# Performance work log

Measured on AMD Instinct MI355X. Metric: run time of the kernel, lower is better.

The kernel has to match this reference:

```python
import jax, jax.numpy as jnp
import numpy as np

HIDDEN = 2048
NUM_HEADS = 16
NUM_KV_HEADS = 4
HEAD_DIM = 128
ROPE_BASE = 10000.0


def apply_rope(x):
    # x: [B, H, S, D]; standard half-split RoPE
    B, H, S, D = x.shape
    half = D // 2
    inv_freq = 1.0 / (ROPE_BASE ** (jnp.arange(half, dtype=jnp.float32) / half))
    ang = jnp.arange(S, dtype=jnp.float32)[:, None] * inv_freq[None, :]  # [S, half]
    cos = jnp.cos(ang).astype(x.dtype)
    sin = jnp.sin(ang).astype(x.dtype)
    x1, x2 = x[..., :half], x[..., half:]
    return jnp.concatenate([x1 * cos - x2 * sin, x1 * sin + x2 * cos], axis=-1)


def setup_inputs() -> dict:
    key = jax.random.key(0)
    ks = jax.random.split(key, 6)
    B, S = 2, 2048
    sd = 1.0 / np.sqrt(HIDDEN)
    x = jax.random.normal(ks[0], (B, S, HIDDEN), dtype=jnp.float32)
    wq = jax.random.normal(ks[1], (NUM_HEADS * HEAD_DIM, HIDDEN), dtype=jnp.float32) * sd
    wk = jax.random.normal(ks[2], (NUM_KV_HEADS * HEAD_DIM, HIDDEN), dtype=jnp.float32) * sd
    wv = jax.random.normal(ks[3], (NUM_KV_HEADS * HEAD_DIM, HIDDEN), dtype=jnp.float32) * sd
    wo = jax.random.normal(ks[4], (HIDDEN, NUM_HEADS * HEAD_DIM), dtype=jnp.float32) * sd
    key_weights = jnp.ones((NUM_HEADS,), dtype=jnp.float32)
    return {"x": x, "wq": wq, "wk": wk, "wv": wv, "wo": wo, "key_weights": key_weights}


def reference(x, wq, wk, wv, wo, key_weights):
    B, S, _ = x.shape
    g = NUM_HEADS // NUM_KV_HEADS
    scale = HEAD_DIM ** -0.5
    # projections -> [B, H, S, D]
    q = (x @ wq.T).reshape(B, S, NUM_HEADS, HEAD_DIM).transpose(0, 2, 1, 3)
    k = (x @ wk.T).reshape(B, S, NUM_KV_HEADS, HEAD_DIM).transpose(0, 2, 1, 3)
    v = (x @ wv.T).reshape(B, S, NUM_KV_HEADS, HEAD_DIM).transpose(0, 2, 1, 3)
    q = apply_rope(q)
    k = apply_rope(k)
    # GQA expansion (repeat_interleave over head dim)
    k = jnp.repeat(k, g, axis=1)
    v = jnp.repeat(v, g, axis=1)
    # per-head key scaling fused into K
    k = k * key_weights[None, :, None, None]
    scores = jnp.einsum("bhqd,bhkd->bhqk", q, k) * scale
    causal = jnp.triu(jnp.ones((S, S), dtype=bool), k=1)
    scores = jnp.where(causal, -jnp.inf, scores)
    attn = jax.nn.softmax(scores, axis=-1)
    out = jnp.einsum("bhqk,bhkd->bhqd", attn, v)
    out = out.transpose(0, 2, 1, 3).reshape(B, S, NUM_HEADS * HEAD_DIM)
    return out @ wo.T
```

## Files before the change

### kernel.cpp

```cpp
#include <hip/hip_runtime.h>

#define S_LEN 2048
#define HID 2048
#define NH 16
#define HD 128
#define QKV_N 3072
#define KCOL 2048
#define VCOL 2560

typedef unsigned short ushort_t;
using bf16x8 = __attribute__((ext_vector_type(8))) __bf16;
using f32x4 = __attribute__((ext_vector_type(4))) float;
using ushort8 = __attribute__((ext_vector_type(8))) unsigned short;
using ushort4v = __attribute__((ext_vector_type(4))) unsigned short;

__device__ __forceinline__ unsigned short f2bf(float f) {
  unsigned int u = __float_as_uint(f);
  unsigned int r = u + 0x7FFFu + ((u >> 16) & 1u);
  return (unsigned short)(r >> 16);
}
__device__ __forceinline__ float bf2f(unsigned short h) {
  return __uint_as_float(((unsigned int)h) << 16);
}

__device__ __forceinline__ void gload_lds16(const ushort_t* g, ushort_t* lds) {
  __builtin_amdgcn_global_load_lds(
      (const __attribute__((address_space(1))) unsigned int*)g,
      (__attribute__((address_space(3))) unsigned int*)lds, 16, 0, 0);
}

__global__ void cast_bf16_kernel(const float* __restrict__ in, ushort_t* __restrict__ out, int n4) {
  int i = blockIdx.x * 256 + threadIdx.x;
  if (i >= n4) return;
  float4 v = reinterpret_cast<const float4*>(in)[i];
  ushort4v o;
  o.x = f2bf(v.x); o.y = f2bf(v.y); o.z = f2bf(v.z); o.w = f2bf(v.w);
  reinterpret_cast<ushort4v*>(out)[i] = o;
}

__global__ void rope_table_kernel(float* __restrict__ cosT, float* __restrict__ sinT) {
  int i = blockIdx.x * 256 + threadIdx.x;
  if (i >= S_LEN * 64) return;
  int s = i >> 6, j = i & 63;
  float inv = __expf(-(float)j * (9.210340371976184f / 64.0f));
  float ang = (float)s * inv;
  float sv, cv;
  sincosf(ang, &sv, &cv);
  cosT[i] = cv;
  sinT[i] = sv;
}

__global__ void rope_apply_kernel(ushort_t* __restrict__ base, const float* __restrict__ cosT,
                                  const float* __restrict__ sinT, const float* __restrict__ kw,
                                  int stride, int lognh, float scale, int useKw, int n) {
  int idx = blockIdx.x * 256 + threadIdx.x;
  if (idx >= n) return;
  int row = idx >> lognh;
  int p = idx & ((1 << lognh) - 1);
  int h = p >> 6, j = p & 63;
  int s = row & (S_LEN - 1);
  float c = cosT[(s << 6) + j];
  float sn = sinT[(s << 6) + j];
  long a = (long)row * stride + h * HD;
  float x1 = bf2f(base[a + j]);
  float x2 = bf2f(base[a + j + 64]);
  float wsc = useKw ? (scale * kw[h]) : scale;
  base[a + j] = f2bf((x1 * c - x2 * sn) * wsc);
  base[a + j + 64] = f2bf((x1 * sn + x2 * c) * wsc);
}

__global__ __launch_bounds__(256) void transpose_v_kernel(const ushort_t* __restrict__ qkv,
                                                          ushort_t* __restrict__ vt) {
  __shared__ ushort_t T[64][76];
  int bid = blockIdx.x;
  int dd = bid & 7;
  int tt = bid >> 3;
  int tid = threadIdx.x;
#pragma unroll
  for (int it = 0; it < 2; ++it) {
    int c = tid + it * 256;
    int i = c >> 3, j8 = c & 7;
    ushort8 v = *reinterpret_cast<const ushort8*>(
        qkv + (long)(tt * 64 + i) * QKV_N + VCOL + dd * 64 + j8 * 8);
    *reinterpret_cast<ushort8*>(&T[i][j8 * 8]) = v;
  }
  __syncthreads();
#pragma unroll
  for (int it = 0; it < 2; ++it) {
    int c = tid + it * 256;
    int jd = c >> 3, sc = c & 7;
    ushort8 o;
#pragma unroll
    for (int e = 0; e < 8; ++e) o[e] = T[sc * 8 + e][jd];
    int token = tt * 64 + sc * 8;
    int b = token >> 11, s = token & (S_LEN - 1);
    int vd = dd * 64 + jd;
    *reinterpret_cast<ushort8*>(vt + ((long)(b * 512 + vd) << 11) + s) = o;
  }
}

__device__ __forceinline__ void store_c(ushort_t* p, float v) { *p = f2bf(v); }
__device__ __forceinline__ void store_c(float* p, float v) { *p = v; }

template <typename OT>
__global__ __launch_bounds__(256) void gemm_bt_kernel(const ushort_t* __restrict__ A,
                                                      const ushort_t* __restrict__ W,
                                                      OT* __restrict__ C, int M, int N, int K) {
  __shared__ ushort_t As[128 * 32];
  __shared__ ushort_t Bs[128 * 32];
  const int tid = threadIdx.x;
  const int l = tid & 63, w = tid >> 6;
  const int wr = w >> 1, wc = w & 1;
  const int r = l & 15, g = l >> 4;
  const long arow0 = (long)blockIdx.y * 128;
  const long brow0 = (long)blockIdx.x * 128;

  f32x4 acc[4][4] = {};

  const int c0 = tid, c1 = tid + 256;
  const ushort_t* a_src0 = A + (arow0 + (c0 >> 2)) * K + ((c0 & 3) << 3);
  const ushort_t* a_src1 = A + (arow0 + (c1 >> 2)) * K + ((c1 & 3) << 3);
  const ushort_t* b_src0 = W + (brow0 + (c0 >> 2)) * K + ((c0 & 3) << 3);
  const ushort_t* b_src1 = W + (brow0 + (c1 >> 2)) * K + ((c1 & 3) << 3);
  ushort_t* a_dst0 = &As[c0 * 8];
  ushort_t* a_dst1 = &As[c1 * 8];
  ushort_t* b_dst0 = &Bs[c0 * 8];
  ushort_t* b_dst1 = &Bs[c1 * 8];

  for (int kk = 0; kk < K; kk += 32) {
    gload_lds16(a_src0 + kk, a_dst0);
    gload_lds16(a_src1 + kk, a_dst1);
    gload_lds16(b_src0 + kk, b_dst0);
    gload_lds16(b_src1 + kk, b_dst1);
    __syncthreads();
    bf16x8 af[4], bw[4];
#pragma unroll
    for (int mi = 0; mi < 4; ++mi)
      af[mi] = *reinterpret_cast<const bf16x8*>(&As[(wr * 64 + mi * 16 + r) * 32 + g * 8]);
#pragma unroll
    for (int ni = 0; ni < 4; ++ni)
      bw[ni] = *reinterpret_cast<const bf16x8*>(&Bs[(wc * 64 + ni * 16 + r) * 32 + g * 8]);
#pragma unroll
    for (int mi = 0; mi < 4; ++mi)
#pragma unroll
      for (int ni = 0; ni < 4; ++ni)
        acc[mi][ni] = __builtin_amdgcn_mfma_f32_16x16x32_bf16(af[mi], bw[ni], acc[mi][ni], 0, 0, 0);
    __syncthreads();
  }

#pragma unroll
  for (int mi = 0; mi < 4; ++mi)
#pragma unroll
    for (int ni = 0; ni < 4; ++ni) {
      int col = (int)brow0 + wc * 64 + ni * 16 + r;
#pragma unroll
      for (int j = 0; j < 4; ++j) {
        int row = (int)arow0 + wr * 64 + mi * 16 + g * 4 + j;
        store_c(&C[(long)row * N + col], acc[mi][ni][j]);
      }
    }
}

__global__ __launch_bounds__(256) void flash_attn_kernel(const ushort_t* __restrict__ qkv,
                                                         const ushort_t* __restrict__ Vt,
                                                         ushort_t* __restrict__ AO) {
  __shared__ ushort_t Ks[64 * 128];
  __shared__ ushort_t Vts[128 * 64];
  __shared__ ushort_t Ps[4][16 * 68];

  const int bid = blockIdx.x;
  const int pr = bid & 15;
  const int h = (bid >> 4) & 15;
  const int b = bid >> 8;
  const int tid = threadIdx.x;
  const int l = tid & 63, w = tid >> 6;
  const int r = l & 15, g = l >> 4;
  const int kvh = h >> 2;

  const ushort_t* Qb = qkv + (long)b * S_LEN * QKV_N + h * HD;
  const ushort_t* Kb = qkv + (long)b * S_LEN * QKV_N + KCOL + kvh * HD;
  const ushort_t* Vb = Vt + ((long)(b * 512 + kvh * HD) << 11);

  for (int pi = 0; pi < 2; ++pi) {
    const int qt = pi ? (31 - pr) : pr;
    const int qg = qt * 64 + w * 16;
    const long qrow0 = (long)b * S_LEN + qg;

    bf16x8 qa[4];
#pragma unroll
    for (int ks = 0; ks < 4; ++ks)
      qa[ks] = *reinterpret_cast<const bf16x8*>(Qb + (long)(qg + r) * QKV_N + ks * 32 + g * 8);

    f32x4 acc[8] = {};
    float mrow[4], lrow[4];
#pragma unroll
    for (int j = 0; j < 4; ++j) { mrow[j] = -1e30f; lrow[j] = 0.f; }

    for (int kv = 0; kv <= qt; ++kv) {
      __syncthreads();
#pragma unroll
      for (int i = 0; i < 4; ++i) {
        int c = tid + i * 256;
        int krow = c >> 4, cc = c & 15;
        int scc = cc ^ (krow & 7);
        gload_lds16(Kb + (long)(kv * 64 + krow) * QKV_N + scc * 8, &Ks[c * 8]);
      }
#pragma unroll
      for (int i = 0; i < 4; ++i) {
        int c = tid + i * 256;
        int vrow = c >> 3, cc = c & 7;
        int scc = cc ^ (vrow & 7);
        gload_lds16(Vb + ((long)vrow << 11) + kv * 64 + scc * 8, &Vts[c * 8]);
      }
      __syncthreads();

      f32x4 s[4] = {};
#pragma unroll
      for (int ks = 0; ks < 4; ++ks) {
        bf16x8 kf[4];
#pragma unroll
        for (int ni = 0; ni < 4; ++ni) {
          int n = ni * 16 + r;
          int chunk = (ks * 4 + g) ^ (n & 7);
          kf[ni] = *reinterpret_cast<const bf16x8*>(
              reinterpret_cast<const char*>(Ks) + n * 256 + chunk * 16);
        }
#pragma unroll
        for (int ni = 0; ni < 4; ++ni)
          s[ni] = __builtin_amdgcn_mfma_f32_16x16x32_bf16(qa[ks], kf[ni], s[ni], 0, 0, 0);
      }
      if (kv == qt) {
#pragma unroll
        for (int ni = 0; ni < 4; ++ni) {
          int key = kv * 64 + ni * 16 + r;
#pragma unroll
          for (int j = 0; j < 4; ++j) {
            int rowq = qg + g * 4 + j;
            if (key > rowq) s[ni][j] = -1e30f;
          }
        }
      }
#pragma unroll
      for (int j = 0; j < 4; ++j) {
        float mx = fmaxf(fmaxf(s[0][j], s[1][j]), fmaxf(s[2][j], s[3][j]));
        mx = fmaxf(mx, __shfl_xor(mx, 1));
        mx = fmaxf(mx, __shfl_xor(mx, 2));
        mx = fmaxf(mx, __shfl_xor(mx, 4));
        mx = fmaxf(mx, __shfl_xor(mx, 8));
        float mo = mrow[j];
        float mn = fmaxf(mo, mx);
        float ef = __expf(mo - mn);
        mrow[j] = mn;
        float psum = 0.f;
#pragma unroll
        for (int ni = 0; ni < 4; ++ni) {
          float p = __expf(s[ni][j] - mn);
          s[ni][j] = p;
          psum += p;
        }
        lrow[j] = lrow[j] * ef + psum;
#pragma unroll
        for (int ni = 0; ni < 8; ++ni) acc[ni][j] *= ef;
      }
#pragma unroll
      for (int ni = 0; ni < 4; ++ni)
#pragma unroll
        for (int j = 0; j < 4; ++j)
          Ps[w][(g * 4 + j) * 68 + ni * 16 + r] = f2bf(s[ni][j]);
#pragma unroll
      for (int ks2 = 0; ks2 < 2; ++ks2) {
        bf16x8 pa = *reinterpret_cast<const bf16x8*>(&Ps[w][r * 68 + ks2 * 32 + g * 8]);
#pragma unroll
        for (int ni = 0; ni < 8; ++ni) {
          int d = ni * 16 + r;
          int chunk = (ks2 * 4 + g) ^ (d & 7);
          bf16x8 vf = *reinterpret_cast<const bf16x8*>(
              reinterpret_cast<const char*>(Vts) + d * 128 + chunk * 16);
          acc[ni] = __builtin_amdgcn_mfma_f32_16x16x32_bf16(pa, vf, acc[ni], 0, 0, 0);
        }
      }
    }

#pragma unroll
    for (int j = 0; j < 4; ++j) {
      float lt = lrow[j];
      lt += __shfl_xor(lt, 1);
      lt += __shfl_xor(lt, 2);
      lt += __shfl_xor(lt, 4);
      lt += __shfl_xor(lt, 8);
      float inv = 1.0f / lt;
#pragma unroll
      for (int ni = 0; ni < 8; ++ni) acc[ni][j] *= inv;
    }
#pragma unroll
    for (int ni = 0; ni < 8; ++ni) {
      int col = h * HD + ni * 16 + r;
#pragma unroll
      for (int j = 0; j < 4; ++j) {
        long row = qrow0 + g * 4 + j;
        AO[row * HID + col] = f2bf(acc[ni][j]);
      }
    }
    __syncthreads();
  }
}

extern "C" void kernel_launch(void* const* d_in, const int* in_sizes, int n_in,
                              void* d_out, int out_size, void* d_ws, size_t ws_size,
                              hipStream_t stream) {
  const float* x = (const float*)d_in[0];
  const float* wq = (const float*)d_in[1];
  const float* wk = (const float*)d_in[2];
  const float* wv = (const float*)d_in[3];
  const float* wo = (const float*)d_in[4];
  const float* kw = (const float*)d_in[5];
  float* out = (float*)d_out;

  ushort_t* ws = (ushort_t*)d_ws;
  ushort_t* xb = ws;
  ushort_t* qkv = xb + 8388608;
  ushort_t* vt = qkv + 12582912;
  ushort_t* wqkv = vt + 2097152;
  float* cosT = (float*)(wqkv + 6291456);
  float* sinT = cosT + S_LEN * 64;

  cast_bf16_kernel<<<8192, 256, 0, stream>>>(x, xb, 2097152);
  cast_bf16_kernel<<<4096, 256, 0, stream>>>(wq, wqkv, 1048576);
  cast_bf16_kernel<<<1024, 256, 0, stream>>>(wk, wqkv + 2048 * 2048, 262144);
  cast_bf16_kernel<<<1024, 256, 0, stream>>>(wv, wqkv + 2560 * 2048, 262144);
  rope_table_kernel<<<512, 256, 0, stream>>>(cosT, sinT);

  gemm_bt_kernel<ushort_t><<<dim3(24, 32), 256, 0, stream>>>(xb, wqkv, qkv, 4096, QKV_N, 2048);

  rope_apply_kernel<<<16384, 256, 0, stream>>>(qkv, cosT, sinT, kw, QKV_N, 10,
                                               0.08838834764831845f, 1, 4194304);
  rope_apply_kernel<<<4096, 256, 0, stream>>>(qkv + KCOL, cosT, sinT, kw, QKV_N, 8,
                                              1.0f, 0, 1048576);

  transpose_v_kernel<<<512, 256, 0, stream>>>(qkv, vt);

  ushort_t* wob = wqkv;
  cast_bf16_kernel<<<4096, 256, 0, stream>>>(wo, wob, 1048576);

  flash_attn_kernel<<<512, 256, 0, stream>>>(qkv, vt, xb);

  gemm_bt_kernel<float><<<dim3(16, 32), 256, 0, stream>>>(xb, wob, out, 4096, 2048, 2048);
}
```

Before: 349.4 us.

## Double-buffer K/V tiles in flash attention and remap blocks across XCDs

Stages K and V tiles into two LDS buffers so the next tile's global-to-LDS load is issued before computing on the current tile, leaving one barrier per iteration instead of two. It also replaces the padded P scratch with an XOR-swizzled layout and remaps the block index so related heads and batches are grouped per XCD for L2 reuse. The extra buffers raise LDS use, which may reduce the number of resident blocks per CU.

```diff
diff --git a/kernel.cpp b/kernel.cpp
--- a/kernel.cpp
+++ b/kernel.cpp
@@ -161,17 +161,38 @@
     }
 }
 
+__device__ __forceinline__ void stage_tile(const ushort_t* __restrict__ Kb,
+                                           const ushort_t* __restrict__ Vb, int kv,
+                                           ushort_t* __restrict__ KsBuf,
+                                           ushort_t* __restrict__ VtsBuf, int tid) {
+#pragma unroll
+  for (int i = 0; i < 4; ++i) {
+    int c = tid + i * 256;
+    int krow = c >> 4, cc = c & 15;
+    int scc = cc ^ (krow & 7);
+    gload_lds16(Kb + (long)(kv * 64 + krow) * QKV_N + scc * 8, &KsBuf[c * 8]);
+  }
+#pragma unroll
+  for (int i = 0; i < 4; ++i) {
+    int c = tid + i * 256;
+    int vrow = c >> 3, cc = c & 7;
+    int scc = cc ^ (vrow & 7);
+    gload_lds16(Vb + ((long)vrow << 11) + kv * 64 + scc * 8, &VtsBuf[c * 8]);
+  }
+}
+
 __global__ __launch_bounds__(256) void flash_attn_kernel(const ushort_t* __restrict__ qkv,
                                                          const ushort_t* __restrict__ Vt,
                                                          ushort_t* __restrict__ AO) {
-  __shared__ ushort_t Ks[64 * 128];
-  __shared__ ushort_t Vts[128 * 64];
-  __shared__ ushort_t Ps[4][16 * 68];
-
-  const int bid = blockIdx.x;
-  const int pr = bid & 15;
-  const int h = (bid >> 4) & 15;
-  const int b = bid >> 8;
+  __shared__ ushort_t Ks[2][64 * 128];
+  __shared__ ushort_t Vts[2][128 * 64];
+  __shared__ ushort_t Ps[4][16 * 64];
+
+  const int d = blockIdx.x;
+  const int o = (d & 7) * 64 + (d >> 3);
+  const int pr = o & 15;
+  const int h = (o >> 4) & 15;
+  const int b = o >> 8;
   const int tid = threadIdx.x;
   const int l = tid & 63, w = tid >> 6;
   const int r = l & 15, g = l >> 4;
@@ -196,23 +217,14 @@
 #pragma unroll
     for (int j = 0; j < 4; ++j) { mrow[j] = -1e30f; lrow[j] = 0.f; }
 
+    stage_tile(Kb, Vb, 0, Ks[0], Vts[0], tid);
+    __syncthreads();
+    int cur = 0;
+
     for (int kv = 0; kv <= qt; ++kv) {
-      __syncthreads();
-#pragma unroll
-      for (int i = 0; i < 4; ++i) {
-        int c = tid + i * 256;
-        int krow = c >> 4, cc = c & 15;
-        int scc = cc ^ (krow & 7);
-        gload_lds16(Kb + (long)(kv * 64 + krow) * QKV_N + scc * 8, &Ks[c * 8]);
-      }
-#pragma unroll
-      for (int i = 0; i < 4; ++i) {
-        int c = tid + i * 256;
-        int vrow = c >> 3, cc = c & 7;
-        int scc = cc ^ (vrow & 7);
-        gload_lds16(Vb + ((long)vrow << 11) + kv * 64 + scc * 8, &Vts[c * 8]);
-      }
-      __syncthreads();
+      if (kv < qt) stage_tile(Kb, Vb, kv + 1, Ks[cur ^ 1], Vts[cur ^ 1], tid);
+      const ushort_t* KsC = Ks[cur];
+      const ushort_t* VtsC = Vts[cur];
 
       f32x4 s[4] = {};
 #pragma unroll
@@ -223,7 +235,7 @@
           int n = ni * 16 + r;
           int chunk = (ks * 4 + g) ^ (n & 7);
           kf[ni] = *reinterpret_cast<const bf16x8*>(
-              reinterpret_cast<const char*>(Ks) + n * 256 + chunk * 16);
+              reinterpret_cast<const char*>(KsC) + n * 256 + chunk * 16);
         }
 #pragma unroll
         for (int ni = 0; ni < 4; ++ni)
@@ -265,20 +277,26 @@
 #pragma unroll
       for (int ni = 0; ni < 4; ++ni)
 #pragma unroll
-        for (int j = 0; j < 4; ++j)
-          Ps[w][(g * 4 + j) * 68 + ni * 16 + r] = f2bf(s[ni][j]);
+        for (int j = 0; j < 4; ++j) {
+          int row = g * 4 + j;
+          int chunk = (ni * 2 + (r >> 3)) ^ (row & 7);
+          Ps[w][row * 64 + chunk * 8 + (r & 7)] = f2bf(s[ni][j]);
+        }
 #pragma unroll
       for (int ks2 = 0; ks2 < 2; ++ks2) {
-        bf16x8 pa = *reinterpret_cast<const bf16x8*>(&Ps[w][r * 68 + ks2 * 32 + g * 8]);
+        bf16x8 pa = *reinterpret_cast<const bf16x8*>(
+            &Ps[w][r * 64 + (((ks2 * 4 + g) ^ (r & 7)) << 3)]);
 #pragma unroll
         for (int ni = 0; ni < 8; ++ni) {
-          int d = ni * 16 + r;
-          int chunk = (ks2 * 4 + g) ^ (d & 7);
+          int dd = ni * 16 + r;
+          int chunk = (ks2 * 4 + g) ^ (dd & 7);
           bf16x8 vf = *reinterpret_cast<const bf16x8*>(
-              reinterpret_cast<const char*>(Vts) + d * 128 + chunk * 16);
+              reinterpret_cast<const char*>(VtsC) + dd * 128 + chunk * 16);
           acc[ni] = __builtin_amdgcn_mfma_f32_16x16x32_bf16(pa, vf, acc[ni], 0, 0, 0);
         }
       }
+      __syncthreads();
+      cur ^= 1;
     }
 
 #pragma unroll
@@ -301,7 +319,6 @@
         AO[row * HID + col] = f2bf(acc[ni][j]);
       }
     }
-    __syncthreads();
   }
 }
 
```

Result: no change. 352.8 us (+1.0%).
